# Kernel optimization log

Hardware: AMD Instinct MI355X
Metric: run time of the kernel (lower is better)

## Reference

```python
import jax, jax.numpy as jnp
import numpy as np

N_NODES = 50000
N_EDGES = 800000
IN_DIM = 128
HID_DIM = 256
OUT_DIM = 5
BATCH = 50000  # batch_size in module; view(batch_size, 5)


def _sage_conv(x, src, dst, Wl, bl, Wr):
    # PyG SAGEConv (aggr='mean', root_weight=True, normalize=False):
    #   out = lin_l(mean_{j in N(i)} x_j) + lin_r(x_i)
    msgs = x[src]                                            # [E, d]
    agg = jax.ops.segment_sum(msgs, dst, num_segments=N_NODES)
    cnt = jax.ops.segment_sum(jnp.ones((src.shape[0],), x.dtype), dst,
                              num_segments=N_NODES)          # [N]
    mean = agg / jnp.maximum(cnt, 1.0)[:, None]              # 0 for isolated nodes
    return mean @ Wl.T + bl + x @ Wr.T


def setup_inputs() -> dict:
    key = jax.random.key(0)
    ks = jax.random.split(key, 8)
    x = jax.random.normal(ks[0], (N_NODES, IN_DIM), dtype=jnp.float32)
    edge_index = jax.random.randint(ks[1], (2, N_EDGES), 0, N_NODES, dtype=jnp.int64)
    s1 = 1.0 / np.sqrt(IN_DIM)
    s2 = 1.0 / np.sqrt(HID_DIM)
    W1l = jax.random.uniform(ks[2], (HID_DIM, IN_DIM), jnp.float32, -s1, s1)
    b1l = jax.random.uniform(ks[3], (HID_DIM,), jnp.float32, -s1, s1)
    W1r = jax.random.uniform(ks[4], (HID_DIM, IN_DIM), jnp.float32, -s1, s1)
    W2l = jax.random.uniform(ks[5], (OUT_DIM, HID_DIM), jnp.float32, -s2, s2)
    b2l = jax.random.uniform(ks[6], (OUT_DIM,), jnp.float32, -s2, s2)
    W2r = jax.random.uniform(ks[7], (OUT_DIM, HID_DIM), jnp.float32, -s2, s2)
    return {"x": x, "edge_index": edge_index,
            "W1l": W1l, "b1l": b1l, "W1r": W1r,
            "W2l": W2l, "b2l": b2l, "W2r": W2r}


def reference(x, edge_index, W1l, b1l, W1r, W2l, b2l, W2r):
    src, dst = edge_index[0], edge_index[1]
    h = jax.nn.relu(_sage_conv(x, src, dst, W1l, b1l, W1r))   # [N, hidden]
    h = jax.nn.relu(_sage_conv(h, src, dst, W2l, b2l, W2r))   # [N, out]
    return h.reshape(BATCH, 5)
```

## Files before the change

### kernel.cpp

```cpp
#include <hip/hip_runtime.h>

static constexpr int NN = 50000;
static constexpr int NE = 800000;
static constexpr int D0 = 128;
static constexpr int D1 = 256;
static constexpr int D2 = 5;

static constexpr int BSZ   = 512;
static constexpr int NBUK  = (NN + BSZ - 1) / BSZ;
static constexpr int CAP   = 9216;
static constexpr int CB    = 400;
static constexpr int CHUNK = 2000;

static constexpr int XB = (NN * 32 + 255) / 256;
static constexpr int WB = (D1 * 64) / 256;
static constexpr int PB = 4;

using short8  = __attribute__((ext_vector_type(8))) short;
using floatx4 = __attribute__((ext_vector_type(4))) float;

__device__ __forceinline__ unsigned short f2b(float f) {
  union { float f; unsigned u; } v; v.f = f;
  unsigned r = v.u + 0x7fffu + ((v.u >> 16) & 1u);
  return (unsigned short)(r >> 16);
}
__device__ __forceinline__ float b2f(unsigned short s) {
  union { unsigned u; float f; } v; v.u = ((unsigned)s) << 16;
  return v.f;
}

__global__ __launch_bounds__(256) void k_prepA(
    const float* __restrict__ x, unsigned short* __restrict__ ab,
    const float* __restrict__ W1l, const float* __restrict__ W1r,
    unsigned short* __restrict__ wb, const float* __restrict__ W2l,
    const float* __restrict__ W2r, unsigned short* __restrict__ w2b,
    const int* __restrict__ src, const int* __restrict__ dst,
    int* __restrict__ gcur, uint2* __restrict__ slab) {
  __shared__ int hist[128], bstart[128], gbase[128], hcur[128], sscan[128];
  __shared__ uint2 pairs[CHUNK];
  const int b = blockIdx.x, t = threadIdx.x;
  if (b < CB) {
    const int e0 = b * CHUNK;
    if (t < 128) hist[t] = 0;
    __syncthreads();
    for (int j = t; j < CHUNK; j += 256)
      atomicAdd(&hist[dst[e0 + j] >> 9], 1);
    __syncthreads();
    if (t < 128) sscan[t] = hist[t];
    __syncthreads();
    for (int dd = 1; dd < 128; dd <<= 1) {
      int u = (t >= dd && t < 128) ? sscan[t - dd] : 0;
      __syncthreads();
      if (t < 128) sscan[t] += u;
      __syncthreads();
    }
    if (t < 128) {
      bstart[t] = sscan[t] - hist[t];
      gbase[t] = (t < NBUK && hist[t] > 0) ? atomicAdd(&gcur[t], hist[t]) : 0;
      hcur[t] = 0;
    }
    __syncthreads();
    for (int j = t; j < CHUNK; j += 256) {
      const int s = src[e0 + j], d = dst[e0 + j];
      const int bk = d >> 9;
      const int pos = bstart[bk] + atomicAdd(&hcur[bk], 1);
      pairs[pos] = make_uint2((unsigned)s, (unsigned)d);
    }
    __syncthreads();
    for (int j = t; j < CHUNK; j += 256) {
      const uint2 pr = pairs[j];
      const int bk = (int)pr.y >> 9;
      slab[(size_t)bk * CAP + gbase[bk] + (j - bstart[bk])] = pr;
    }
    return;
  }
  if (b < CB + XB) {
    int idx = (b - CB) * 256 + t;
    if (idx < NN * 32) {
      int node = idx >> 5, cg = idx & 31;
      float4 v = *(const float4*)(x + (size_t)node * D0 + cg * 4);
      ushort4 o;
      o.x = f2b(v.x); o.y = f2b(v.y); o.z = f2b(v.z); o.w = f2b(v.w);
      *(ushort4*)(ab + (size_t)node * 256 + 128 + cg * 4) = o;
    }
    return;
  }
  if (b < CB + XB + WB) {
    int idx = (b - CB - XB) * 256 + t;
    int c = idx >> 6, k = (idx & 63) * 4;
    const float* srcp = (k < 128) ? (W1l + (size_t)c * 128 + k)
                                  : (W1r + (size_t)c * 128 + (k - 128));
    float4 v = *(const float4*)srcp;
    ushort4 o;
    o.x = f2b(v.x); o.y = f2b(v.y); o.z = f2b(v.z); o.w = f2b(v.w);
    *(ushort4*)(wb + (size_t)c * 256 + k) = o;
    return;
  }
  {
    int idx = (b - CB - XB - WB) * 256 + t;
    int n = idx >> 6, k = (idx & 63) * 4;
    float4 v = {0.f, 0.f, 0.f, 0.f};
    if (n < 5) v = *(const float4*)(W2l + (size_t)n * D1 + k);
    else if (n < 10) v = *(const float4*)(W2r + (size_t)(n - 5) * D1 + k);
    ushort4 o;
    o.x = f2b(v.x); o.y = f2b(v.y); o.z = f2b(v.z); o.w = f2b(v.w);
    *(ushort4*)(w2b + (size_t)n * 256 + k) = o;
  }
}

__global__ __launch_bounds__(512) void k_bucketBC(
    const uint2* __restrict__ slab, const int* __restrict__ gcur,
    int* __restrict__ cur, float* __restrict__ inv,
    int* __restrict__ esort) {
  __shared__ int cnt[BSZ], s[BSZ], lcur[BSZ], g[128];
  const int b = blockIdx.x, t = threadIdx.x;
  const int n0 = b << 9;
  cnt[t] = 0;
  if (t < 128) g[t] = (t < NBUK) ? gcur[t] : 0;
  __syncthreads();
  for (int dd = 1; dd < 128; dd <<= 1) {
    int u = (t >= dd && t < 128) ? g[t - dd] : 0;
    __syncthreads();
    if (t < 128) g[t] += u;
    __syncthreads();
  }
  const int bbase = (b == 0) ? 0 : g[b - 1];
  const int cntE = gcur[b];
  const uint2* sp = slab + (size_t)b * CAP;
  for (int j = t; j < cntE; j += 512)
    atomicAdd(&cnt[(int)sp[j].y - n0], 1);
  __syncthreads();
  s[t] = cnt[t];
  __syncthreads();
  for (int dd = 1; dd < BSZ; dd <<= 1) {
    int u = (t >= dd) ? s[t - dd] : 0;
    __syncthreads();
    s[t] += u;
    __syncthreads();
  }
  const int start = bbase + (s[t] - cnt[t]);
  const int node = n0 + t;
  if (node < NN) {
    cur[node] = start;
    inv[node] = 1.0f / (float)max(cnt[t], 1);
  }
  lcur[t] = start;
  if (b == NBUK - 1 && t == 0) cur[NN] = NE;
  __syncthreads();
  for (int j = t; j < cntE; j += 512) {
    const uint2 pr = sp[j];
    const int p = atomicAdd(&lcur[(int)pr.y - n0], 1);
    esort[p] = (int)pr.x;
  }
}

__global__ __launch_bounds__(256) void k_agg1(
    unsigned short* __restrict__ ab, const int* __restrict__ esort,
    const int* __restrict__ cur, const float* __restrict__ inv) {
  const int i = (blockIdx.x * 256 + threadIdx.x) >> 6;
  const int lane = threadIdx.x & 63;
  if (i >= NN) return;
  int e = cur[i];
  const int end = cur[i + 1];
  float a0 = 0.f, b0 = 0.f, a1 = 0.f, b1 = 0.f;
  float a2 = 0.f, b2 = 0.f, a3 = 0.f, b3 = 0.f;
  const unsigned short* xb = ab + 128 + lane * 2;
  while (e < end && (e & 3)) {
    const unsigned v = *(const unsigned*)(xb + (size_t)esort[e] * 256);
    a0 += b2f((unsigned short)v); b0 += b2f((unsigned short)(v >> 16));
    ++e;
  }
  for (; e + 7 < end; e += 8) {
    const int4 s0 = *(const int4*)(esort + e);
    const int4 s1 = *(const int4*)(esort + e + 4);
    const unsigned v0 = *(const unsigned*)(xb + (size_t)s0.x * 256);
    const unsigned v1 = *(const unsigned*)(xb + (size_t)s0.y * 256);
    const unsigned v2 = *(const unsigned*)(xb + (size_t)s0.z * 256);
    const unsigned v3 = *(const unsigned*)(xb + (size_t)s0.w * 256);
    const unsigned v4 = *(const unsigned*)(xb + (size_t)s1.x * 256);
    const unsigned v5 = *(const unsigned*)(xb + (size_t)s1.y * 256);
    const unsigned v6 = *(const unsigned*)(xb + (size_t)s1.z * 256);
    const unsigned v7 = *(const unsigned*)(xb + (size_t)s1.w * 256);
    a0 += b2f((unsigned short)v0); b0 += b2f((unsigned short)(v0 >> 16));
    a1 += b2f((unsigned short)v1); b1 += b2f((unsigned short)(v1 >> 16));
    a2 += b2f((unsigned short)v2); b2 += b2f((unsigned short)(v2 >> 16));
    a3 += b2f((unsigned short)v3); b3 += b2f((unsigned short)(v3 >> 16));
    a0 += b2f((unsigned short)v4); b0 += b2f((unsigned short)(v4 >> 16));
    a1 += b2f((unsigned short)v5); b1 += b2f((unsigned short)(v5 >> 16));
    a2 += b2f((unsigned short)v6); b2 += b2f((unsigned short)(v6 >> 16));
    a3 += b2f((unsigned short)v7); b3 += b2f((unsigned short)(v7 >> 16));
  }
  if (e + 3 < end) {
    const int4 s0 = *(const int4*)(esort + e);
    const unsigned v0 = *(const unsigned*)(xb + (size_t)s0.x * 256);
    const unsigned v1 = *(const unsigned*)(xb + (size_t)s0.y * 256);
    const unsigned v2 = *(const unsigned*)(xb + (size_t)s0.z * 256);
    const unsigned v3 = *(const unsigned*)(xb + (size_t)s0.w * 256);
    a0 += b2f((unsigned short)v0); b0 += b2f((unsigned short)(v0 >> 16));
    a1 += b2f((unsigned short)v1); b1 += b2f((unsigned short)(v1 >> 16));
    a2 += b2f((unsigned short)v2); b2 += b2f((unsigned short)(v2 >> 16));
    a3 += b2f((unsigned short)v3); b3 += b2f((unsigned short)(v3 >> 16));
    e += 4;
  }
  for (; e < end; ++e) {
    const unsigned v = *(const unsigned*)(xb + (size_t)esort[e] * 256);
    a0 += b2f((unsigned short)v); b0 += b2f((unsigned short)(v >> 16));
  }
  const float sc = inv[i];
  const float sa = (a0 + a1) + (a2 + a3);
  const float sb = (b0 + b1) + (b2 + b3);
  const unsigned out =
      ((unsigned)f2b(sb * sc) << 16) | (unsigned)f2b(sa * sc);
  *(unsigned*)(ab + (size_t)i * 256 + lane * 2) = out;
}

__global__ __launch_bounds__(256) void k_gemm1f(
    const unsigned short* __restrict__ ab, const unsigned short* __restrict__ wb,
    const unsigned short* __restrict__ w2b, const float* __restrict__ b1l,
    float* __restrict__ tt, float* __restrict__ rp) {
  __shared__ short sAB[2 * 128 * 72];
  short* sA = sAB;
  short* sB = sAB + 128 * 72;
  const int tid = threadIdx.x;
  const int row0 = blockIdx.y * 128;
  const int hf = blockIdx.x;
  const int col0 = hf * 128;
  const int wave = tid >> 6, lane = tid & 63;
  const int quad = lane >> 4, m16 = lane & 15;
  const int wm = wave & 1, wn = wave >> 1;
  const int lr = tid >> 2;
  const int lk = (tid & 3) * 8;

  floatx4 acc[4][4];
#pragma unroll
  for (int a = 0; a < 4; ++a)
#pragma unroll
    for (int b = 0; b < 4; ++b) acc[a][b] = {0.f, 0.f, 0.f, 0.f};

  const int gr0 = row0 + lr, gr1 = row0 + lr + 64;
  const bool ok0 = gr0 < NN, ok1 = gr1 < NN;
  const unsigned short* aptr0 = ab + (size_t)gr0 * 256 + lk;
  const unsigned short* aptr1 = ab + (size_t)gr1 * 256 + lk;
  const unsigned short* bptr0 = wb + (size_t)(col0 + lr) * 256 + lk;
  const unsigned short* bptr1 = wb + (size_t)(col0 + lr + 64) * 256 + lk;
  short* sA0 = &sA[lr * 72 + lk];
  short* sA1 = &sA[(lr + 64) * 72 + lk];
  short* sB0 = &sB[lr * 72 + lk];
  short* sB1 = &sB[(lr + 64) * 72 + lk];
  const uint4 zz = make_uint4(0, 0, 0, 0);

  uint4 a00 = ok0 ? *(const uint4*)(aptr0) : zz;
  uint4 a01 = ok0 ? *(const uint4*)(aptr0 + 32) : zz;
  uint4 a10 = ok1 ? *(const uint4*)(aptr1) : zz;
  uint4 a11 = ok1 ? *(const uint4*)(aptr1 + 32) : zz;
  uint4 b00 = *(const uint4*)(bptr0);
  uint4 b01 = *(const uint4*)(bptr0 + 32);
  uint4 b10 = *(const uint4*)(bptr1);
  uint4 b11 = *(const uint4*)(bptr1 + 32);

  for (int kk = 0; kk < 256; kk += 64) {
    __syncthreads();
    *(uint4*)sA0 = a00;
    *(uint4*)(sA0 + 32) = a01;
    *(uint4*)sA1 = a10;
    *(uint4*)(sA1 + 32) = a11;
    *(uint4*)sB0 = b00;
    *(uint4*)(sB0 + 32) = b01;
    *(uint4*)sB1 = b10;
    *(uint4*)(sB1 + 32) = b11;
    __syncthreads();
    if (kk < 192) {
      const int kn = kk + 64;
      a00 = ok0 ? *(const uint4*)(aptr0 + kn) : zz;
      a01 = ok0 ? *(const uint4*)(aptr0 + kn + 32) : zz;
      a10 = ok1 ? *(const uint4*)(aptr1 + kn) : zz;
      a11 = ok1 ? *(const uint4*)(aptr1 + kn + 32) : zz;
      b00 = *(const uint4*)(bptr0 + kn);
      b01 = *(const uint4*)(bptr0 + kn + 32);
      b10 = *(const uint4*)(bptr1 + kn);
      b11 = *(const uint4*)(bptr1 + kn + 32);
    }
#pragma unroll
    for (int ko = 0; ko < 64; ko += 32) {
      short8 af[4], bf[4];
#pragma unroll
      for (int mt = 0; mt < 4; ++mt)
        af[mt] =
            *(const short8*)&sA[(wm * 64 + mt * 16 + m16) * 72 + ko + quad * 8];
#pragma unroll
      for (int nt = 0; nt < 4; ++nt)
        bf[nt] =
            *(const short8*)&sB[(wn * 64 + nt * 16 + m16) * 72 + ko + quad * 8];
#pragma unroll
      for (int mt = 0; mt < 4; ++mt)
#pragma unroll
        for (int nt = 0; nt < 4; ++nt)
          acc[mt][nt] = __builtin_amdgcn_mfma_f32_16x16x32_bf16(
              af[mt], bf[nt], acc[mt][nt], 0, 0, 0);
    }
  }

  __syncthreads();
  short* sH = sAB;
#pragma unroll
  for (int nt = 0; nt < 4; ++nt) {
    const int cl = wn * 64 + nt * 16 + m16;
    const float bias = b1l[col0 + cl];
#pragma unroll
    for (int mt = 0; mt < 4; ++mt)
#pragma unroll
      for (int rg = 0; rg < 4; ++rg) {
        const int rl = wm * 64 + mt * 16 + quad * 4 + rg;
        sH[rl * 136 + cl] = (short)f2b(fmaxf(acc[mt][nt][rg] + bias, 0.f));
      }
  }
  __syncthreads();
  floatx4 c2[2] = {{0.f, 0.f, 0.f, 0.f}, {0.f, 0.f, 0.f, 0.f}};
#pragma unroll
  for (int kb = 0; kb < 4; ++kb) {
    const short8 bf2 =
        *(const short8*)&w2b[m16 * 256 + col0 + kb * 32 + quad * 8];
#pragma unroll
    for (int i = 0; i < 2; ++i) {
      const int mrow = (wave * 2 + i) * 16 + m16;
      const short8 af2 = *(const short8*)&sH[mrow * 136 + kb * 32 + quad * 8];
      c2[i] = __builtin_amdgcn_mfma_f32_16x16x32_bf16(af2, bf2, c2[i], 0, 0, 0);
    }
  }
#pragma unroll
  for (int i = 0; i < 2; ++i) {
    const int rbase = row0 + (wave * 2 + i) * 16 + quad * 4;
#pragma unroll
    for (int rg = 0; rg < 4; ++rg) {
      const int row = rbase + rg;
      if (row < NN) {
        if (m16 < 5)
          tt[(size_t)row * 16 + hf * 8 + m16] = c2[i][rg];
        else if (m16 < 10)
          rp[(size_t)hf * ((size_t)NN * 8) + (size_t)row * 8 + (m16 - 5)] =
              c2[i][rg];
      }
    }
  }
}

__global__ __launch_bounds__(256) void k_layer2(
    const float* __restrict__ tt, const float* __restrict__ rp,
    const int* __restrict__ esort, const int* __restrict__ cur,
    const float* __restrict__ inv, const float* __restrict__ b2l,
    float* __restrict__ out) {
  const int node = blockIdx.x * 16 + (threadIdx.x >> 4);
  const int l = threadIdx.x & 15;
  if (node >= NN) return;
  const int beg = cur[node], end = cur[node + 1];
  float s0 = 0.f, s1 = 0.f, s2 = 0.f, s3 = 0.f, s4 = 0.f;
  for (int e = beg + l; e < end; e += 16) {
    const float* tp = tt + (size_t)esort[e] * 16;
    const float4 p0 = *(const float4*)tp;
    const float q0 = tp[4];
    const float4 p1 = *(const float4*)(tp + 8);
    const float q1 = tp[12];
    s0 += p0.x + p1.x;
    s1 += p0.y + p1.y;
    s2 += p0.z + p1.z;
    s3 += p0.w + p1.w;
    s4 += q0 + q1;
  }
#pragma unroll
  for (int m = 1; m < 16; m <<= 1) {
    s0 += __shfl_xor(s0, m, 64);
    s1 += __shfl_xor(s1, m, 64);
    s2 += __shfl_xor(s2, m, 64);
    s3 += __shfl_xor(s3, m, 64);
    s4 += __shfl_xor(s4, m, 64);
  }
  if (l == 0) {
    const float sc = inv[node];
    const float* r0 = rp + (size_t)node * 8;
    const float* r1 = rp + (size_t)NN * 8 + (size_t)node * 8;
    out[(size_t)node * D2 + 0] = fmaxf(s0 * sc + b2l[0] + r0[0] + r1[0], 0.f);
    out[(size_t)node * D2 + 1] = fmaxf(s1 * sc + b2l[1] + r0[1] + r1[1], 0.f);
    out[(size_t)node * D2 + 2] = fmaxf(s2 * sc + b2l[2] + r0[2] + r1[2], 0.f);
    out[(size_t)node * D2 + 3] = fmaxf(s3 * sc + b2l[3] + r0[3] + r1[3], 0.f);
    out[(size_t)node * D2 + 4] = fmaxf(s4 * sc + b2l[4] + r0[4] + r1[4], 0.f);
  }
}

extern "C" void kernel_launch(void* const* d_in, const int* in_sizes, int n_in,
                              void* d_out, int out_size, void* d_ws,
                              size_t ws_size, hipStream_t stream) {
  const float* x   = (const float*)d_in[0];
  const int*   ei  = (const int*)d_in[1];
  const int*   src = ei;
  const int*   dst = ei + NE;
  const float* W1l = (const float*)d_in[2];
  const float* b1l = (const float*)d_in[3];
  const float* W1r = (const float*)d_in[4];
  const float* W2l = (const float*)d_in[5];
  const float* b2l = (const float*)d_in[6];
  const float* W2r = (const float*)d_in[7];
  float* out = (float*)d_out;

  unsigned short* ab  = (unsigned short*)d_ws;
  unsigned short* wb  = ab + (size_t)NN * 256;
  unsigned short* w2b = wb + 256 * 256;
  float* tt   = (float*)(w2b + 16 * 256);
  float* rp   = tt + (size_t)NN * 16;
  uint2* slab = (uint2*)(rp + (size_t)NN * 16);
  int*   gcur = (int*)(slab + (size_t)NBUK * CAP);
  int*   cur  = gcur + 128;
  int*   esort = cur + NN + 1;
  float* inv  = (float*)(esort + NE);

  hipMemsetAsync(gcur, 0, 128 * sizeof(int), stream);

  k_prepA<<<CB + XB + WB + PB, 256, 0, stream>>>(x, ab, W1l, W1r, wb, W2l, W2r,
                                                 w2b, src, dst, gcur, slab);
  k_bucketBC<<<NBUK, 512, 0, stream>>>(slab, gcur, cur, inv, esort);
  k_agg1<<<(NN * 64 + 255) / 256, 256, 0, stream>>>(ab, esort, cur, inv);
  dim3 g1(2, (NN + 127) / 128);
  k_gemm1f<<<g1, 256, 0, stream>>>(ab, wb, w2b, b1l, tt, rp);
  k_layer2<<<(NN + 15) / 16, 256, 0, stream>>>(tt, rp, esort, cur, inv, b2l,
                                               out);
}
```

Baseline: 179.9 us.

## Split bf16 features into quarter planes for cache-local neighbor aggregation

Writes a second copy of the bf16 input features split into four 32-column planes, and has the layer-1 aggregation process one plane per block. Each gather row is then 64 bytes and each plane's working set is a quarter the size, which is meant to improve L2/MALL hit rates for random neighbor reads. Bucket size for the edge sort is halved to 256 nodes, so more blocks with single-pass scans share the work. Nontemporal loads and stores are used for the index stream and the output. This costs an extra write of the feature matrix and four passes over the edge list.

```diff
diff --git a/kernel.cpp b/kernel.cpp
--- a/kernel.cpp
+++ b/kernel.cpp
@@ -6,9 +6,9 @@
 static constexpr int D1 = 256;
 static constexpr int D2 = 5;
 
-static constexpr int BSZ   = 512;
+static constexpr int BSZ   = 256;
 static constexpr int NBUK  = (NN + BSZ - 1) / BSZ;
-static constexpr int CAP   = 9216;
+static constexpr int CAP   = 4800;
 static constexpr int CB    = 400;
 static constexpr int CHUNK = 2000;
 
@@ -18,6 +18,7 @@
 
 using short8  = __attribute__((ext_vector_type(8))) short;
 using floatx4 = __attribute__((ext_vector_type(4))) float;
+using intx4   = __attribute__((ext_vector_type(4))) int;
 
 __device__ __forceinline__ unsigned short f2b(float f) {
   union { float f; unsigned u; } v; v.f = f;
@@ -35,41 +36,40 @@
     unsigned short* __restrict__ wb, const float* __restrict__ W2l,
     const float* __restrict__ W2r, unsigned short* __restrict__ w2b,
     const int* __restrict__ src, const int* __restrict__ dst,
-    int* __restrict__ gcur, uint2* __restrict__ slab) {
-  __shared__ int hist[128], bstart[128], gbase[128], hcur[128], sscan[128];
+    int* __restrict__ gcur, uint2* __restrict__ slab,
+    unsigned short* __restrict__ xq) {
+  __shared__ int hist[256], bstart[256], gbase[256], hcur[256], sscan[256];
   __shared__ uint2 pairs[CHUNK];
   const int b = blockIdx.x, t = threadIdx.x;
   if (b < CB) {
     const int e0 = b * CHUNK;
-    if (t < 128) hist[t] = 0;
+    hist[t] = 0;
     __syncthreads();
     for (int j = t; j < CHUNK; j += 256)
-      atomicAdd(&hist[dst[e0 + j] >> 9], 1);
-    __syncthreads();
-    if (t < 128) sscan[t] = hist[t];
-    __syncthreads();
-    for (int dd = 1; dd < 128; dd <<= 1) {
-      int u = (t >= dd && t < 128) ? sscan[t - dd] : 0;
+      atomicAdd(&hist[dst[e0 + j] >> 8], 1);
+    __syncthreads();
+    sscan[t] = hist[t];
+    __syncthreads();
+    for (int dd = 1; dd < 256; dd <<= 1) {
+      int u = (t >= dd) ? sscan[t - dd] : 0;
       __syncthreads();
-      if (t < 128) sscan[t] += u;
+      sscan[t] += u;
       __syncthreads();
     }
-    if (t < 128) {
-      bstart[t] = sscan[t] - hist[t];
-      gbase[t] = (t < NBUK && hist[t] > 0) ? atomicAdd(&gcur[t], hist[t]) : 0;
-      hcur[t] = 0;
-    }
+    bstart[t] = sscan[t] - hist[t];
+    gbase[t] = (t < NBUK && hist[t] > 0) ? atomicAdd(&gcur[t], hist[t]) : 0;
+    hcur[t] = 0;
     __syncthreads();
     for (int j = t; j < CHUNK; j += 256) {
       const int s = src[e0 + j], d = dst[e0 + j];
-      const int bk = d >> 9;
+      const int bk = d >> 8;
       const int pos = bstart[bk] + atomicAdd(&hcur[bk], 1);
       pairs[pos] = make_uint2((unsigned)s, (unsigned)d);
     }
     __syncthreads();
     for (int j = t; j < CHUNK; j += 256) {
       const uint2 pr = pairs[j];
-      const int bk = (int)pr.y >> 9;
+      const int bk = (int)pr.y >> 8;
       slab[(size_t)bk * CAP + gbase[bk] + (j - bstart[bk])] = pr;
     }
     return;
@@ -82,6 +82,9 @@
       ushort4 o;
       o.x = f2b(v.x); o.y = f2b(v.y); o.z = f2b(v.z); o.w = f2b(v.w);
       *(ushort4*)(ab + (size_t)node * 256 + 128 + cg * 4) = o;
+      const int q = cg >> 3;
+      *(ushort4*)(xq + (size_t)q * ((size_t)NN * 32) + (size_t)node * 32 +
+                  (cg & 7) * 4) = o;
     }
     return;
   }
@@ -108,26 +111,26 @@
   }
 }
 
-__global__ __launch_bounds__(512) void k_bucketBC(
+__global__ __launch_bounds__(256) void k_bucketBC(
     const uint2* __restrict__ slab, const int* __restrict__ gcur,
     int* __restrict__ cur, float* __restrict__ inv,
     int* __restrict__ esort) {
-  __shared__ int cnt[BSZ], s[BSZ], lcur[BSZ], g[128];
+  __shared__ int cnt[BSZ], s[BSZ], lcur[BSZ], g[256];
   const int b = blockIdx.x, t = threadIdx.x;
-  const int n0 = b << 9;
+  const int n0 = b << 8;
   cnt[t] = 0;
-  if (t < 128) g[t] = (t < NBUK) ? gcur[t] : 0;
-  __syncthreads();
-  for (int dd = 1; dd < 128; dd <<= 1) {
-    int u = (t >= dd && t < 128) ? g[t - dd] : 0;
-    __syncthreads();
-    if (t < 128) g[t] += u;
+  g[t] = (t < NBUK) ? gcur[t] : 0;
+  __syncthreads();
+  for (int dd = 1; dd < 256; dd <<= 1) {
+    int u = (t >= dd) ? g[t - dd] : 0;
+    __syncthreads();
+    g[t] += u;
     __syncthreads();
   }
   const int bbase = (b == 0) ? 0 : g[b - 1];
   const int cntE = gcur[b];
   const uint2* sp = slab + (size_t)b * CAP;
-  for (int j = t; j < cntE; j += 512)
+  for (int j = t; j < cntE; j += 256)
     atomicAdd(&cnt[(int)sp[j].y - n0], 1);
   __syncthreads();
   s[t] = cnt[t];
@@ -147,71 +150,44 @@
   lcur[t] = start;
   if (b == NBUK - 1 && t == 0) cur[NN] = NE;
   __syncthreads();
-  for (int j = t; j < cntE; j += 512) {
+  for (int j = t; j < cntE; j += 256) {
     const uint2 pr = sp[j];
     const int p = atomicAdd(&lcur[(int)pr.y - n0], 1);
     esort[p] = (int)pr.x;
   }
 }
 
-__global__ __launch_bounds__(256) void k_agg1(
-    unsigned short* __restrict__ ab, const int* __restrict__ esort,
-    const int* __restrict__ cur, const float* __restrict__ inv) {
-  const int i = (blockIdx.x * 256 + threadIdx.x) >> 6;
+__global__ __launch_bounds__(256) void k_agg1q(
+    const unsigned short* __restrict__ xq, unsigned short* __restrict__ ab,
+    const int* __restrict__ esort, const int* __restrict__ cur,
+    const float* __restrict__ inv) {
+  const int q = blockIdx.x & 3;
+  const int grp = blockIdx.x >> 2;
+  const int wave = threadIdx.x >> 6;
   const int lane = threadIdx.x & 63;
-  if (i >= NN) return;
-  int e = cur[i];
-  const int end = cur[i + 1];
-  float a0 = 0.f, b0 = 0.f, a1 = 0.f, b1 = 0.f;
-  float a2 = 0.f, b2 = 0.f, a3 = 0.f, b3 = 0.f;
-  const unsigned short* xb = ab + 128 + lane * 2;
+  const int node = grp * 8 + wave * 2 + (lane >> 5);
+  if (node >= NN) return;
+  const int d = lane & 31;
+  const unsigned short* __restrict__ xp =
+      xq + (size_t)q * ((size_t)NN * 32) + d;
+  int e = cur[node];
+  const int end = cur[node + 1];
+  float a0 = 0.f, a1 = 0.f, a2 = 0.f, a3 = 0.f;
   while (e < end && (e & 3)) {
-    const unsigned v = *(const unsigned*)(xb + (size_t)esort[e] * 256);
-    a0 += b2f((unsigned short)v); b0 += b2f((unsigned short)(v >> 16));
+    a0 += b2f(xp[(size_t)esort[e] * 32]);
     ++e;
   }
-  for (; e + 7 < end; e += 8) {
-    const int4 s0 = *(const int4*)(esort + e);
-    const int4 s1 = *(const int4*)(esort + e + 4);
-    const unsigned v0 = *(const unsigned*)(xb + (size_t)s0.x * 256);
-    const unsigned v1 = *(const unsigned*)(xb + (size_t)s0.y * 256);
-    const unsigned v2 = *(const unsigned*)(xb + (size_t)s0.z * 256);
-    const unsigned v3 = *(const unsigned*)(xb + (size_t)s0.w * 256);
-    const unsigned v4 = *(const unsigned*)(xb + (size_t)s1.x * 256);
-    const unsigned v5 = *(const unsigned*)(xb + (size_t)s1.y * 256);
-    const unsigned v6 = *(const unsigned*)(xb + (size_t)s1.z * 256);
-    const unsigned v7 = *(const unsigned*)(xb + (size_t)s1.w * 256);
-    a0 += b2f((unsigned short)v0); b0 += b2f((unsigned short)(v0 >> 16));
-    a1 += b2f((unsigned short)v1); b1 += b2f((unsigned short)(v1 >> 16));
-    a2 += b2f((unsigned short)v2); b2 += b2f((unsigned short)(v2 >> 16));
-    a3 += b2f((unsigned short)v3); b3 += b2f((unsigned short)(v3 >> 16));
-    a0 += b2f((unsigned short)v4); b0 += b2f((unsigned short)(v4 >> 16));
-    a1 += b2f((unsigned short)v5); b1 += b2f((unsigned short)(v5 >> 16));
-    a2 += b2f((unsigned short)v6); b2 += b2f((unsigned short)(v6 >> 16));
-    a3 += b2f((unsigned short)v7); b3 += b2f((unsigned short)(v7 >> 16));
-  }
-  if (e + 3 < end) {
-    const int4 s0 = *(const int4*)(esort + e);
-    const unsigned v0 = *(const unsigned*)(xb + (size_t)s0.x * 256);
-    const unsigned v1 = *(const unsigned*)(xb + (size_t)s0.y * 256);
-    const unsigned v2 = *(const unsigned*)(xb + (size_t)s0.z * 256);
-    const unsigned v3 = *(const unsigned*)(xb + (size_t)s0.w * 256);
-    a0 += b2f((unsigned short)v0); b0 += b2f((unsigned short)(v0 >> 16));
-    a1 += b2f((unsigned short)v1); b1 += b2f((unsigned short)(v1 >> 16));
-    a2 += b2f((unsigned short)v2); b2 += b2f((unsigned short)(v2 >> 16));
-    a3 += b2f((unsigned short)v3); b3 += b2f((unsigned short)(v3 >> 16));
-    e += 4;
-  }
-  for (; e < end; ++e) {
-    const unsigned v = *(const unsigned*)(xb + (size_t)esort[e] * 256);
-    a0 += b2f((unsigned short)v); b0 += b2f((unsigned short)(v >> 16));
-  }
-  const float sc = inv[i];
-  const float sa = (a0 + a1) + (a2 + a3);
-  const float sb = (b0 + b1) + (b2 + b3);
-  const unsigned out =
-      ((unsigned)f2b(sb * sc) << 16) | (unsigned)f2b(sa * sc);
-  *(unsigned*)(ab + (size_t)i * 256 + lane * 2) = out;
+  for (; e + 3 < end; e += 4) {
+    const intx4 s4 = __builtin_nontemporal_load((const intx4*)(esort + e));
+    a0 += b2f(xp[(size_t)s4.x * 32]);
+    a1 += b2f(xp[(size_t)s4.y * 32]);
+    a2 += b2f(xp[(size_t)s4.z * 32]);
+    a3 += b2f(xp[(size_t)s4.w * 32]);
+  }
+  for (; e < end; ++e) a0 += b2f(xp[(size_t)esort[e] * 32]);
+  const float m = ((a0 + a1) + (a2 + a3)) * inv[node];
+  __builtin_nontemporal_store(f2b(m),
+                              ab + (size_t)node * 256 + q * 32 + d);
 }
 
 __global__ __launch_bounds__(256) void k_gemm1f(
@@ -408,16 +384,17 @@
   float* rp   = tt + (size_t)NN * 16;
   uint2* slab = (uint2*)(rp + (size_t)NN * 16);
   int*   gcur = (int*)(slab + (size_t)NBUK * CAP);
-  int*   cur  = gcur + 128;
-  int*   esort = cur + NN + 1;
-  float* inv  = (float*)(esort + NE);
-
-  hipMemsetAsync(gcur, 0, 128 * sizeof(int), stream);
+  int*   esort = gcur + 256;
+  int*   cur  = esort + NE;
+  float* inv  = (float*)(cur + NN + 4);
+  unsigned short* xq = (unsigned short*)(inv + NN);
+
+  hipMemsetAsync(gcur, 0, 256 * sizeof(int), stream);
 
   k_prepA<<<CB + XB + WB + PB, 256, 0, stream>>>(x, ab, W1l, W1r, wb, W2l, W2r,
-                                                 w2b, src, dst, gcur, slab);
-  k_bucketBC<<<NBUK, 512, 0, stream>>>(slab, gcur, cur, inv, esort);
-  k_agg1<<<(NN * 64 + 255) / 256, 256, 0, stream>>>(ab, esort, cur, inv);
+                                                 w2b, src, dst, gcur, slab, xq);
+  k_bucketBC<<<NBUK, 256, 0, stream>>>(slab, gcur, cur, inv, esort);
+  k_agg1q<<<4 * ((NN + 7) / 8), 256, 0, stream>>>(xq, ab, esort, cur, inv);
   dim3 g1(2, (NN + 127) / 128);
   k_gemm1f<<<g1, 256, 0, stream>>>(ab, wb, w2b, b1l, tt, rp);
   k_layer2<<<(NN + 15) / 16, 256, 0, stream>>>(tt, rp, esort, cur, inv, b2l,
```

After: 219.4 us. 22.0% more time.

## Shrink buckets, stage sorted edges in LDS, and lane-per-column layer2 gather

Applied to the files above, without the earlier changes.

Halves the bucket size to 256 nodes, which doubles the bucket count and enlarges the prep histograms to 256 entries. The bucket sort now builds the sorted edge list in shared memory and writes it out to global memory in coalesced order, replacing the old scattered global writes. Layer 2 now assigns each of 16 lanes one column of tt and loads the node's edges four at a time with int4 reads. This trades per-lane strided float reads for coalesced row reads. The risk is overflow if a 256-node bucket receives more than 4800 edges; the random inputs average about 4096 per bucket.

```diff
diff --git a/kernel.cpp b/kernel.cpp
--- a/kernel.cpp
+++ b/kernel.cpp
@@ -6,9 +6,9 @@
 static constexpr int D1 = 256;
 static constexpr int D2 = 5;
 
-static constexpr int BSZ   = 512;
+static constexpr int BSZ   = 256;
 static constexpr int NBUK  = (NN + BSZ - 1) / BSZ;
-static constexpr int CAP   = 9216;
+static constexpr int CAP   = 4800;
 static constexpr int CB    = 400;
 static constexpr int CHUNK = 2000;
 
@@ -36,40 +36,38 @@
     const float* __restrict__ W2r, unsigned short* __restrict__ w2b,
     const int* __restrict__ src, const int* __restrict__ dst,
     int* __restrict__ gcur, uint2* __restrict__ slab) {
-  __shared__ int hist[128], bstart[128], gbase[128], hcur[128], sscan[128];
+  __shared__ int hist[256], bstart[256], gbase[256], hcur[256], sscan[256];
   __shared__ uint2 pairs[CHUNK];
   const int b = blockIdx.x, t = threadIdx.x;
   if (b < CB) {
     const int e0 = b * CHUNK;
-    if (t < 128) hist[t] = 0;
+    hist[t] = 0;
     __syncthreads();
     for (int j = t; j < CHUNK; j += 256)
-      atomicAdd(&hist[dst[e0 + j] >> 9], 1);
-    __syncthreads();
-    if (t < 128) sscan[t] = hist[t];
-    __syncthreads();
-    for (int dd = 1; dd < 128; dd <<= 1) {
-      int u = (t >= dd && t < 128) ? sscan[t - dd] : 0;
+      atomicAdd(&hist[dst[e0 + j] >> 8], 1);
+    __syncthreads();
+    sscan[t] = hist[t];
+    __syncthreads();
+    for (int dd = 1; dd < 256; dd <<= 1) {
+      int u = (t >= dd) ? sscan[t - dd] : 0;
       __syncthreads();
-      if (t < 128) sscan[t] += u;
+      sscan[t] += u;
       __syncthreads();
     }
-    if (t < 128) {
-      bstart[t] = sscan[t] - hist[t];
-      gbase[t] = (t < NBUK && hist[t] > 0) ? atomicAdd(&gcur[t], hist[t]) : 0;
-      hcur[t] = 0;
-    }
+    bstart[t] = sscan[t] - hist[t];
+    gbase[t] = (t < NBUK && hist[t] > 0) ? atomicAdd(&gcur[t], hist[t]) : 0;
+    hcur[t] = 0;
     __syncthreads();
     for (int j = t; j < CHUNK; j += 256) {
       const int s = src[e0 + j], d = dst[e0 + j];
-      const int bk = d >> 9;
+      const int bk = d >> 8;
       const int pos = bstart[bk] + atomicAdd(&hcur[bk], 1);
       pairs[pos] = make_uint2((unsigned)s, (unsigned)d);
     }
     __syncthreads();
     for (int j = t; j < CHUNK; j += 256) {
       const uint2 pr = pairs[j];
-      const int bk = (int)pr.y >> 9;
+      const int bk = (int)pr.y >> 8;
       slab[(size_t)bk * CAP + gbase[bk] + (j - bstart[bk])] = pr;
     }
     return;
@@ -108,26 +106,27 @@
   }
 }
 
-__global__ __launch_bounds__(512) void k_bucketBC(
+__global__ __launch_bounds__(256) void k_bucketBC(
     const uint2* __restrict__ slab, const int* __restrict__ gcur,
     int* __restrict__ cur, float* __restrict__ inv,
     int* __restrict__ esort) {
-  __shared__ int cnt[BSZ], s[BSZ], lcur[BSZ], g[128];
+  __shared__ int cnt[BSZ], s[BSZ], lcur[BSZ], g[256];
+  __shared__ int sorted[CAP];
   const int b = blockIdx.x, t = threadIdx.x;
-  const int n0 = b << 9;
+  const int n0 = b << 8;
   cnt[t] = 0;
-  if (t < 128) g[t] = (t < NBUK) ? gcur[t] : 0;
-  __syncthreads();
-  for (int dd = 1; dd < 128; dd <<= 1) {
-    int u = (t >= dd && t < 128) ? g[t - dd] : 0;
-    __syncthreads();
-    if (t < 128) g[t] += u;
+  g[t] = (t < NBUK) ? gcur[t] : 0;
+  __syncthreads();
+  for (int dd = 1; dd < 256; dd <<= 1) {
+    int u = (t >= dd) ? g[t - dd] : 0;
+    __syncthreads();
+    g[t] += u;
     __syncthreads();
   }
   const int bbase = (b == 0) ? 0 : g[b - 1];
   const int cntE = gcur[b];
   const uint2* sp = slab + (size_t)b * CAP;
-  for (int j = t; j < cntE; j += 512)
+  for (int j = t; j < cntE; j += 256)
     atomicAdd(&cnt[(int)sp[j].y - n0], 1);
   __syncthreads();
   s[t] = cnt[t];
@@ -144,14 +143,17 @@
     cur[node] = start;
     inv[node] = 1.0f / (float)max(cnt[t], 1);
   }
-  lcur[t] = start;
+  lcur[t] = s[t] - cnt[t];
   if (b == NBUK - 1 && t == 0) cur[NN] = NE;
   __syncthreads();
-  for (int j = t; j < cntE; j += 512) {
+  for (int j = t; j < cntE; j += 256) {
     const uint2 pr = sp[j];
     const int p = atomicAdd(&lcur[(int)pr.y - n0], 1);
-    esort[p] = (int)pr.x;
-  }
+    sorted[p] = (int)pr.x;
+  }
+  __syncthreads();
+  for (int j = t; j < cntE; j += 256)
+    esort[bbase + j] = sorted[j];
 }
 
 __global__ __launch_bounds__(256) void k_agg1(
@@ -353,36 +355,24 @@
   const int l = threadIdx.x & 15;
   if (node >= NN) return;
   const int beg = cur[node], end = cur[node + 1];
-  float s0 = 0.f, s1 = 0.f, s2 = 0.f, s3 = 0.f, s4 = 0.f;
-  for (int e = beg + l; e < end; e += 16) {
-    const float* tp = tt + (size_t)esort[e] * 16;
-    const float4 p0 = *(const float4*)tp;
-    const float q0 = tp[4];
-    const float4 p1 = *(const float4*)(tp + 8);
-    const float q1 = tp[12];
-    s0 += p0.x + p1.x;
-    s1 += p0.y + p1.y;
-    s2 += p0.z + p1.z;
-    s3 += p0.w + p1.w;
-    s4 += q0 + q1;
-  }
-#pragma unroll
-  for (int m = 1; m < 16; m <<= 1) {
-    s0 += __shfl_xor(s0, m, 64);
-    s1 += __shfl_xor(s1, m, 64);
-    s2 += __shfl_xor(s2, m, 64);
-    s3 += __shfl_xor(s3, m, 64);
-    s4 += __shfl_xor(s4, m, 64);
-  }
-  if (l == 0) {
-    const float sc = inv[node];
-    const float* r0 = rp + (size_t)node * 8;
-    const float* r1 = rp + (size_t)NN * 8 + (size_t)node * 8;
-    out[(size_t)node * D2 + 0] = fmaxf(s0 * sc + b2l[0] + r0[0] + r1[0], 0.f);
-    out[(size_t)node * D2 + 1] = fmaxf(s1 * sc + b2l[1] + r0[1] + r1[1], 0.f);
-    out[(size_t)node * D2 + 2] = fmaxf(s2 * sc + b2l[2] + r0[2] + r1[2], 0.f);
-    out[(size_t)node * D2 + 3] = fmaxf(s3 * sc + b2l[3] + r0[3] + r1[3], 0.f);
-    out[(size_t)node * D2 + 4] = fmaxf(s4 * sc + b2l[4] + r0[4] + r1[4], 0.f);
+  float s = 0.f, u = 0.f;
+  int e = beg;
+  for (; e + 3 < end; e += 4) {
+    const int4 r4 = *(const int4*)(esort + e);
+    const float t0 = tt[(size_t)r4.x * 16 + l];
+    const float t1 = tt[(size_t)r4.y * 16 + l];
+    const float t2 = tt[(size_t)r4.z * 16 + l];
+    const float t3 = tt[(size_t)r4.w * 16 + l];
+    s += t0 + t2;
+    u += t1 + t3;
+  }
+  for (; e < end; ++e) s += tt[(size_t)esort[e] * 16 + l];
+  s += u;
+  s += __shfl_xor(s, 8, 64);
+  if (l < 5) {
+    const float r = rp[(size_t)node * 8 + l] +
+                    rp[(size_t)NN * 8 + (size_t)node * 8 + l];
+    out[(size_t)node * D2 + l] = fmaxf(s * inv[node] + b2l[l] + r, 0.f);
   }
 }
 
@@ -408,15 +398,15 @@
   float* rp   = tt + (size_t)NN * 16;
   uint2* slab = (uint2*)(rp + (size_t)NN * 16);
   int*   gcur = (int*)(slab + (size_t)NBUK * CAP);
-  int*   cur  = gcur + 128;
-  int*   esort = cur + NN + 1;
-  float* inv  = (float*)(esort + NE);
-
-  hipMemsetAsync(gcur, 0, 128 * sizeof(int), stream);
+  int*   esort = gcur + 256;
+  int*   cur  = esort + NE;
+  float* inv  = (float*)(cur + NN + 4);
+
+  hipMemsetAsync(gcur, 0, 256 * sizeof(int), stream);
 
   k_prepA<<<CB + XB + WB + PB, 256, 0, stream>>>(x, ab, W1l, W1r, wb, W2l, W2r,
                                                  w2b, src, dst, gcur, slab);
-  k_bucketBC<<<NBUK, 512, 0, stream>>>(slab, gcur, cur, inv, esort);
+  k_bucketBC<<<NBUK, 256, 0, stream>>>(slab, gcur, cur, inv, esort);
   k_agg1<<<(NN * 64 + 255) / 256, 256, 0, stream>>>(ab, esort, cur, inv);
   dim3 g1(2, (NN + 127) / 128);
   k_gemm1f<<<g1, 256, 0, stream>>>(ab, wb, w2b, b1l, tt, rp);
```

New measurement: 177.8 us. No clear change (-1.2%).
